# Performance work log

Measured on AMD Instinct MI355X. Metric: run time of the kernel, lower is better.

Reference implementation:

```python
import jax, jax.numpy as jnp
import numpy as np

N, E, F_IN, HID, HEADS, B, CLASSES = 50000, 800000, 128, 64, 4, 512, 2


def setup_inputs() -> dict:
    key = jax.random.key(0)
    ks = jax.random.split(key, 20)
    s = 0.05
    inp = {
        "x": jax.random.normal(ks[0], (N, F_IN), jnp.float32),
        "edge_index": jax.random.randint(ks[1], (2, E), 0, N, jnp.int32),
        "batch": jnp.sort(jax.random.randint(ks[2], (N,), 0, B, jnp.int32)),
        # GCN layers (3): layer0 F_IN->HID, layers 1,2 HID->HID
        "gcn_w0": jax.random.normal(ks[3], (F_IN, HID), jnp.float32) * s,
        "gcn_b0": jnp.zeros((HID,), jnp.float32),
        "gcn_w1": jax.random.normal(ks[4], (HID, HID), jnp.float32) * s,
        "gcn_b1": jnp.zeros((HID,), jnp.float32),
        "gcn_w2": jax.random.normal(ks[5], (HID, HID), jnp.float32) * s,
        "gcn_b2": jnp.zeros((HID,), jnp.float32),
        # GAT: W [HID, HEADS*HID], attention vectors [HEADS, HID], bias [HID] (concat=False)
        "gat_w": jax.random.normal(ks[6], (HID, HEADS * HID), jnp.float32) * s,
        "gat_att_src": jax.random.normal(ks[7], (HEADS, HID), jnp.float32) * s,
        "gat_att_dst": jax.random.normal(ks[8], (HEADS, HID), jnp.float32) * s,
        "gat_b": jnp.zeros((HID,), jnp.float32),
        # MLP head
        "lin1_w": jax.random.normal(ks[9], (HID, HID // 2), jnp.float32) * s,
        "lin1_b": jnp.zeros((HID // 2,), jnp.float32),
        "lin2_w": jax.random.normal(ks[10], (HID // 2, CLASSES), jnp.float32) * s,
        "lin2_b": jnp.zeros((CLASSES,), jnp.float32),
    }
    return inp


def _forward(x, edge_index, batch,
             gcn_w0, gcn_b0, gcn_w1, gcn_b1, gcn_w2, gcn_b2,
             gat_w, gat_att_src, gat_att_dst, gat_b,
             lin1_w, lin1_b, lin2_w, lin2_b):
    n = x.shape[0]
    loop = jnp.arange(n, dtype=edge_index.dtype)
    src = jnp.concatenate([edge_index[0], loop])  # [E+N] with self-loops
    dst = jnp.concatenate([edge_index[1], loop])

    # symmetric GCN normalization (self-loops included, deg >= 1)
    deg = jax.ops.segment_sum(jnp.ones_like(dst, dtype=x.dtype), dst, num_segments=n)
    dinv = jax.lax.rsqrt(jnp.maximum(deg, 1.0))
    norm = dinv[src] * dinv[dst]  # [E+N]

    for W, b in ((gcn_w0, gcn_b0), (gcn_w1, gcn_b1), (gcn_w2, gcn_b2)):
        h = x @ W  # [N, HID]
        x = jax.ops.segment_sum(h[src] * norm[:, None], dst, num_segments=n) + b
        x = jax.nn.relu(x)  # dropout is identity in eval mode

    # GAT layer (heads=HEADS, concat=False -> mean over heads)
    H, C = gat_att_src.shape
    h = (x @ gat_w).reshape(n, H, C)  # [N, H, C]
    a_src = jnp.einsum('nhc,hc->nh', h, gat_att_src)
    a_dst = jnp.einsum('nhc,hc->nh', h, gat_att_dst)
    e = jax.nn.leaky_relu(a_src[src] + a_dst[dst], 0.2)  # [E+N, H]
    m = jax.ops.segment_max(e, dst, num_segments=n)      # per-dst softmax max
    p = jnp.exp(e - m[dst])
    denom = jax.ops.segment_sum(p, dst, num_segments=n)
    alpha = p / denom[dst]                                # [E+N, H]
    out = jax.ops.segment_sum(h[src] * alpha[:, :, None], dst, num_segments=n)
    x = jax.nn.relu(out.mean(axis=1) + gat_b)             # [N, HID]

    # global mean pool + global max pool over graphs
    cnt = jax.ops.segment_sum(jnp.ones((n,), x.dtype), batch, num_segments=B)
    mean_p = jax.ops.segment_sum(x, batch, num_segments=B) / jnp.maximum(cnt, 1.0)[:, None]
    max_p = jax.ops.segment_max(x, batch, num_segments=B)
    max_p = jnp.where(cnt[:, None] > 0, max_p, 0.0)
    g = mean_p + max_p  # [B, HID]

    g = jax.nn.relu(g @ lin1_w + lin1_b)
    return g @ lin2_w + lin2_b  # [B, CLASSES]


def reference(x, edge_index, batch,
              gcn_w0, gcn_b0, gcn_w1, gcn_b1, gcn_w2, gcn_b2,
              gat_w, gat_att_src, gat_att_dst, gat_b,
              lin1_w, lin1_b, lin2_w, lin2_b):
    return _forward(x, edge_index, batch,
                    gcn_w0, gcn_b0, gcn_w1, gcn_b1, gcn_w2, gcn_b2,
                    gat_w, gat_att_src, gat_att_dst, gat_b,
                    lin1_w, lin1_b, lin2_w, lin2_b)
```

## Files before the change

kernel.cpp:

```cpp
#include <hip/hip_runtime.h>
#include <math.h>

typedef short bf8 __attribute__((ext_vector_type(8)));
typedef float f4 __attribute__((ext_vector_type(4)));
typedef unsigned short ushort_t;

#define BRANGE 128
#define NB_E 256

__device__ __forceinline__ float lanebcast(float v, int l) {
  return __int_as_float(__builtin_amdgcn_readlane(__float_as_int(v), l));
}
__device__ __forceinline__ int ilanebcast(int v, int l) {
  return __builtin_amdgcn_readlane(v, l);
}

__device__ __forceinline__ float wave_sum(float v) {
#pragma unroll
  for (int off = 32; off > 0; off >>= 1) v += __shfl_xor(v, off, 64);
  return v;
}

__device__ __forceinline__ ushort_t f2bf(float x) {
  unsigned int u = __float_as_uint(x);
  return (ushort_t)((u + 0x7fffu + ((u >> 16) & 1u)) >> 16);
}
__device__ __forceinline__ float b2f(ushort_t h) {
  return __uint_as_float(((unsigned int)h) << 16);
}


__global__ __launch_bounds__(256) void k_ehist(const int* __restrict__ dst,
                                               int* __restrict__ bhistT, int E, int nbuk) {
  __shared__ int h[512];
  int b = blockIdx.x, tid = threadIdx.x;
  for (int i = tid; i < nbuk; i += 256) h[i] = 0;
  __syncthreads();
  int chunk = (E + gridDim.x - 1) / gridDim.x;
  int e0 = b * chunk, e1 = min(E, e0 + chunk);
  for (int e = e0 + tid; e < e1; e += 256) atomicAdd(&h[dst[e] >> 7], 1);
  __syncthreads();
  for (int i = tid; i < nbuk; i += 256) bhistT[i * NB_E + b] = h[i];
}

__global__ __launch_bounds__(256) void k_btot(const int* __restrict__ bhistT,
                                              int* __restrict__ bcnt, int nb) {
  __shared__ int sm[256];
  int b = blockIdx.x, tid = threadIdx.x;
  sm[tid] = (tid < nb) ? bhistT[b * NB_E + tid] : 0;
  __syncthreads();
  for (int off = 128; off > 0; off >>= 1) {
    if (tid < off) sm[tid] += sm[tid + off];
    __syncthreads();
  }
  if (tid == 0) bcnt[b] = sm[0];
}

__global__ __launch_bounds__(512) void k_bscan(
    const int* __restrict__ bcnt, int* __restrict__ edgebase, int nbuk,
    int* __restrict__ rowstart, int n, int E) {
  __shared__ int smem[512];
  int t = threadIdx.x;
  int v = (t < nbuk) ? bcnt[t] : 0;
  smem[t] = v;
  __syncthreads();
  for (int off = 1; off < 512; off <<= 1) {
    int u = (t >= off) ? smem[t - off] : 0;
    __syncthreads();
    smem[t] += u;
    __syncthreads();
  }
  if (t < nbuk) edgebase[t] = smem[t] - v;
  if (t == 0) rowstart[n] = E + n;
}

__global__ __launch_bounds__(256) void k_bbase(int* __restrict__ bhistT,
                                               const int* __restrict__ edgebase,
                                               int nb) {
  __shared__ int sm[256];
  int b = blockIdx.x, tid = threadIdx.x;
  int v = (tid < nb) ? bhistT[b * NB_E + tid] : 0;
  sm[tid] = v;
  __syncthreads();
  for (int off = 1; off < 256; off <<= 1) {
    int u = (tid >= off) ? sm[tid - off] : 0;
    __syncthreads();
    sm[tid] += u;
    __syncthreads();
  }
  if (tid < nb) bhistT[b * NB_E + tid] = edgebase[b] + sm[tid] - v;
}

__global__ __launch_bounds__(256) void k_ebucket(
    const int* __restrict__ es, const int* __restrict__ ed,
    const int* __restrict__ bhistT, int* __restrict__ bedges, int E, int nbuk) {
  __shared__ int cur[512];
  int b = blockIdx.x, tid = threadIdx.x;
  for (int i = tid; i < nbuk; i += 256) cur[i] = bhistT[i * NB_E + b];
  __syncthreads();
  int chunk = (E + gridDim.x - 1) / gridDim.x;
  int e0 = b * chunk, e1 = min(E, e0 + chunk);
  for (int e = e0 + tid; e < e1; e += 256) {
    int s = es[e], d = ed[e];
    int pos = atomicAdd(&cur[d >> 7], 1);
    bedges[pos] = (s << 7) | (d & 127);
  }
}

__global__ __launch_bounds__(256) void k_ebsort(
    const int* __restrict__ bedges, const int* __restrict__ edgebase,
    const int* __restrict__ bcnt, int* __restrict__ colidx,
    int* __restrict__ rowstart, float* __restrict__ dinv, int n) {
  __shared__ int h[128];
  __shared__ int c[128];
  int b = blockIdx.x, tid = threadIdx.x;
  int nodes0 = b * BRANGE;
  int nnode = min(BRANGE, n - nodes0);
  int ebase = edgebase[b], ecnt = bcnt[b];
  int colbase = ebase + nodes0;
  if (tid < 128) h[tid] = (tid < nnode) ? 1 : 0;
  __syncthreads();
  for (int k = ebase + tid; k < ebase + ecnt; k += 256)
    atomicAdd(&h[bedges[k] & 127], 1);
  __syncthreads();
  int own = (tid < 128) ? h[tid] : 0;
  for (int off = 1; off < 128; off <<= 1) {
    int t = (tid >= off && tid < 128) ? h[tid - off] : 0;
    __syncthreads();
    if (tid < 128) h[tid] += t;
    __syncthreads();
  }
  if (tid < nnode) {
    int excl = h[tid] - own;
    int node = nodes0 + tid;
    rowstart[node] = colbase + excl;
    dinv[node] = 1.0f / sqrtf((float)own);
    colidx[colbase + excl] = node;
    c[tid] = excl + 1;
  }
  __syncthreads();
  for (int k = ebase + tid; k < ebase + ecnt; k += 256) {
    int p = bedges[k];
    int pos = atomicAdd(&c[p & 127], 1);
    colidx[colbase + pos] = p >> 7;
  }
}


__global__ void k_wswz0(const float* __restrict__ W, ushort_t* __restrict__ Bh,
                        ushort_t* __restrict__ Bl) {
  int e = blockIdx.x * 256 + threadIdx.x;
  if (e >= 4 * 4 * 64) return;
  int lane = e & 63, kc = (e >> 6) & 3, ct = e >> 8;
  int k0 = kc * 32 + (lane >> 4) * 8;
  int col = ct * 16 + (lane & 15);
#pragma unroll
  for (int j = 0; j < 8; j++) {
    float w = W[(k0 + j) * 64 + col];
    ushort_t h = f2bf(w);
    Bh[(size_t)e * 8 + j] = h;
    Bl[(size_t)e * 8 + j] = f2bf(w - b2f(h));
  }
}

__global__ void k_wswzg(const float* __restrict__ W, ushort_t* __restrict__ Bh,
                        ushort_t* __restrict__ Bl) {
  int e = blockIdx.x * 256 + threadIdx.x;
  if (e >= 4 * 8 * 64) return;
  int lane = e & 63, kc = (e >> 6) & 7, ct = e >> 9;
  int k0 = kc * 32 + (lane >> 4) * 8;
  int col = ct * 16 + (lane & 15);
#pragma unroll
  for (int j = 0; j < 8; j++) {
    int k = k0 + j;
    float w = W[(k & 63) * 256 + (k >> 6) * 64 + col];
    ushort_t h = f2bf(w);
    Bh[(size_t)e * 8 + j] = h;
    Bl[(size_t)e * 8 + j] = f2bf(w - b2f(h));
  }
}

__global__ __launch_bounds__(256) void k_gemm0_mfma(
    const float* __restrict__ X, const ushort_t* __restrict__ Bh,
    const ushort_t* __restrict__ Bl, const float* __restrict__ dinv,
    ushort_t* __restrict__ H, int n, int ntiles) {
  int tid = threadIdx.x, lane = tid & 63, wave = tid >> 6;
  int m = lane & 15, q = lane >> 4;
  for (int tile = blockIdx.x * 4 + wave; tile < ntiles; tile += gridDim.x * 4) {
    int ra = tile * 16 + m;
    if (ra >= n) ra = n - 1;
    const float* xrow = X + (size_t)ra * 128;
    f4 acc[4];
#pragma unroll
    for (int ct = 0; ct < 4; ct++) acc[ct] = (f4){0.f, 0.f, 0.f, 0.f};
#pragma unroll 2
    for (int kc = 0; kc < 4; kc++) {
      int ko = kc * 32 + q * 8;
      float4 xa = *(const float4*)(xrow + ko);
      float4 xb = *(const float4*)(xrow + ko + 4);
      float f[8] = {xa.x, xa.y, xa.z, xa.w, xb.x, xb.y, xb.z, xb.w};
      union { ushort_t u[8]; bf8 v; } Uh, Ul;
#pragma unroll
      for (int j = 0; j < 8; j++) {
        ushort_t h = f2bf(f[j]);
        Uh.u[j] = h;
        Ul.u[j] = f2bf(f[j] - b2f(h));
      }
#pragma unroll
      for (int ct = 0; ct < 4; ct++) {
        size_t boff = ((size_t)(ct * 4 + kc) * 64 + lane) * 8;
        bf8 bh = *(const bf8*)(Bh + boff);
        bf8 bl = *(const bf8*)(Bl + boff);
        acc[ct] = __builtin_amdgcn_mfma_f32_16x16x32_bf16(Uh.v, bh, acc[ct], 0, 0, 0);
        acc[ct] = __builtin_amdgcn_mfma_f32_16x16x32_bf16(Ul.v, bh, acc[ct], 0, 0, 0);
        acc[ct] = __builtin_amdgcn_mfma_f32_16x16x32_bf16(Uh.v, bl, acc[ct], 0, 0, 0);
      }
    }
#pragma unroll
    for (int r = 0; r < 4; r++) {
      int row = tile * 16 + q * 4 + r;
      if (row < n) {
        float dv = dinv[row];
#pragma unroll
        for (int ct = 0; ct < 4; ct++)
          H[(size_t)row * 64 + ct * 16 + m] = f2bf(acc[ct][r] * dv);
      }
    }
  }
}

__device__ __forceinline__ float gather_sum(const ushort_t* __restrict__ h_in,
                                            const int* __restrict__ colidx,
                                            int s0, int s1, int lane) {
  float acc = 0.0f, accB = 0.0f;
  for (int base = s0; base < s1; base += 64) {
    int cnt = min(64, s1 - base);
    int myidx = (lane < cnt) ? colidx[base + lane] : 0;
    int k = 0;
    for (; k + 3 < cnt; k += 4) {
      int sa = ilanebcast(myidx, k);
      int sb = ilanebcast(myidx, k + 1);
      int sc = ilanebcast(myidx, k + 2);
      int sd = ilanebcast(myidx, k + 3);
      float va = b2f(h_in[(size_t)sa * 64 + lane]);
      float vb = b2f(h_in[(size_t)sb * 64 + lane]);
      float vc = b2f(h_in[(size_t)sc * 64 + lane]);
      float vd = b2f(h_in[(size_t)sd * 64 + lane]);
      acc += va; accB += vb; acc += vc; accB += vd;
    }
    for (; k < cnt; k++) {
      int sa = ilanebcast(myidx, k);
      acc += b2f(h_in[(size_t)sa * 64 + lane]);
    }
  }
  return acc + accB;
}

__global__ __launch_bounds__(256) void k_agg_gemm(
    const ushort_t* __restrict__ h_in, const float* __restrict__ dinv,
    const int* __restrict__ rowstart, const int* __restrict__ colidx,
    const float* __restrict__ bias, const float* __restrict__ Wn,
    ushort_t* __restrict__ h_out, int n) {
  __shared__ float lds_w[64 * 64];
  int tid = threadIdx.x;
  for (int idx = tid; idx < 64 * 64; idx += 256) lds_w[idx] = Wn[idx];
  __syncthreads();
  int lane = tid & 63;
  float bv = bias[lane];
  int gw = blockIdx.x * 4 + (tid >> 6);
  int nw = gridDim.x * 4;
  for (int node = gw; node < n; node += nw) {
    int s0 = rowstart[node], s1 = rowstart[node + 1];
    float acc = gather_sum(h_in, colidx, s0, s1, lane);
    float dvn = dinv[node];
    float x1 = fmaxf(fmaf(dvn, acc, bv), 0.0f);
    float o = 0.0f;
#pragma unroll 8
    for (int k = 0; k < 64; k++)
      o = fmaf(lanebcast(x1, k), lds_w[k * 64 + lane], o);
    h_out[(size_t)node * 64 + lane] = f2bf(o * dvn);
  }
}

__global__ __launch_bounds__(256) void k_agg_gatpre(
    const ushort_t* __restrict__ h_in, const float* __restrict__ dinv,
    const int* __restrict__ rowstart, const int* __restrict__ colidx,
    const float* __restrict__ bias,
    const float* __restrict__ q_src, const float* __restrict__ q_dst,
    ushort_t* __restrict__ x3, float* __restrict__ a_src, float* __restrict__ a_dst,
    int n) {
  int tid = threadIdx.x;
  int lane = tid & 63;
  float bv = bias[lane];
  float qs[4], qd[4];
#pragma unroll
  for (int h = 0; h < 4; h++) {
    qs[h] = q_src[h * 64 + lane];
    qd[h] = q_dst[h * 64 + lane];
  }
  int gw = blockIdx.x * 4 + (tid >> 6);
  int nw = gridDim.x * 4;
  for (int node = gw; node < n; node += nw) {
    int s0 = rowstart[node], s1 = rowstart[node + 1];
    float acc = gather_sum(h_in, colidx, s0, s1, lane);
    float xv = fmaxf(fmaf(dinv[node], acc, bv), 0.0f);
    x3[(size_t)node * 64 + lane] = f2bf(xv);
    float ps[4], pd[4];
#pragma unroll
    for (int h = 0; h < 4; h++) {
      ps[h] = wave_sum(xv * qs[h]);
      pd[h] = wave_sum(xv * qd[h]);
    }
    if (lane == 0) {
      *(float4*)&a_src[(size_t)node * 4] = make_float4(ps[0], ps[1], ps[2], ps[3]);
      *(float4*)&a_dst[(size_t)node * 4] = make_float4(pd[0], pd[1], pd[2], pd[3]);
    }
  }
}

__global__ void k_qpre(const float* __restrict__ W, const float* __restrict__ att_s,
                       const float* __restrict__ att_d,
                       float* __restrict__ q_src, float* __restrict__ q_dst) {
  int t = threadIdx.x;
  int h = t >> 6, k = t & 63;
  float ss = 0.0f, sd = 0.0f;
  for (int c = 0; c < 64; c++) {
    float w = W[k * 256 + h * 64 + c];
    ss = fmaf(w, att_s[h * 64 + c], ss);
    sd = fmaf(w, att_d[h * 64 + c], sd);
  }
  q_src[h * 64 + k] = ss;
  q_dst[h * 64 + k] = sd;
}

__global__ __launch_bounds__(256) void k_gat_gather(
    const ushort_t* __restrict__ x3, const float* __restrict__ a_src,
    const float* __restrict__ a_dst, const int* __restrict__ rowstart,
    const int* __restrict__ colidx, ushort_t* __restrict__ Ahi,
    ushort_t* __restrict__ Alo, int n) {
  int node = (blockIdx.x * blockDim.x + threadIdx.x) >> 6;
  int lane = threadIdx.x & 63;
  if (node >= n) return;
  const float4 adv = *(const float4*)&a_dst[(size_t)node * 4];
  int s0 = rowstart[node], s1 = rowstart[node + 1];
  float acc0 = 0, acc1 = 0, acc2 = 0, acc3 = 0;
  float S0 = 0, S1 = 0, S2 = 0, S3 = 0;
  for (int base = s0; base < s1; base += 64) {
    int cnt = min(64, s1 - base);
    bool act = (lane < cnt);
    int myidx = act ? colidx[base + lane] : 0;
    float w0 = 0, w1 = 0, w2 = 0, w3 = 0;
    if (act) {
      const float4 as = *(const float4*)&a_src[(size_t)myidx * 4];
      float e0 = as.x + adv.x; e0 = (e0 > 0.f) ? e0 : 0.2f * e0; w0 = __expf(e0);
      float e1 = as.y + adv.y; e1 = (e1 > 0.f) ? e1 : 0.2f * e1; w1 = __expf(e1);
      float e2 = as.z + adv.z; e2 = (e2 > 0.f) ? e2 : 0.2f * e2; w2 = __expf(e2);
      float e3 = as.w + adv.w; e3 = (e3 > 0.f) ? e3 : 0.2f * e3; w3 = __expf(e3);
    }
    S0 += wave_sum(w0); S1 += wave_sum(w1);
    S2 += wave_sum(w2); S3 += wave_sum(w3);
    int k = 0;
    for (; k + 1 < cnt; k += 2) {
      int sa = ilanebcast(myidx, k);
      int sb = ilanebcast(myidx, k + 1);
      float wa0 = lanebcast(w0, k), wb0 = lanebcast(w0, k + 1);
      float wa1 = lanebcast(w1, k), wb1 = lanebcast(w1, k + 1);
      float wa2 = lanebcast(w2, k), wb2 = lanebcast(w2, k + 1);
      float wa3 = lanebcast(w3, k), wb3 = lanebcast(w3, k + 1);
      float va = b2f(x3[(size_t)sa * 64 + lane]);
      float vb = b2f(x3[(size_t)sb * 64 + lane]);
      acc0 = fmaf(wa0, va, acc0); acc1 = fmaf(wa1, va, acc1);
      acc2 = fmaf(wa2, va, acc2); acc3 = fmaf(wa3, va, acc3);
      acc0 = fmaf(wb0, vb, acc0); acc1 = fmaf(wb1, vb, acc1);
      acc2 = fmaf(wb2, vb, acc2); acc3 = fmaf(wb3, vb, acc3);
    }
    if (k < cnt) {
      int sa = ilanebcast(myidx, k);
      float wa0 = lanebcast(w0, k), wa1 = lanebcast(w1, k);
      float wa2 = lanebcast(w2, k), wa3 = lanebcast(w3, k);
      float va = b2f(x3[(size_t)sa * 64 + lane]);
      acc0 = fmaf(wa0, va, acc0); acc1 = fmaf(wa1, va, acc1);
      acc2 = fmaf(wa2, va, acc2); acc3 = fmaf(wa3, va, acc3);
    }
  }
  float v[4] = {acc0 * (0.25f / S0), acc1 * (0.25f / S1),
                acc2 * (0.25f / S2), acc3 * (0.25f / S3)};
  size_t baseo = (size_t)node * 256 + lane;
#pragma unroll
  for (int h = 0; h < 4; h++) {
    ushort_t hb = f2bf(v[h]);
    Ahi[baseo + h * 64] = hb;
    Alo[baseo + h * 64] = f2bf(v[h] - b2f(hb));
  }
}

__global__ __launch_bounds__(256) void k_gat_proj_mfma(
    const ushort_t* __restrict__ Ahi, const ushort_t* __restrict__ Alo,
    const ushort_t* __restrict__ Bh, const ushort_t* __restrict__ Bl,
    const float* __restrict__ bias, float* __restrict__ out, int n, int ntiles) {
  int tid = threadIdx.x, lane = tid & 63, wave = tid >> 6;
  int m = lane & 15, q = lane >> 4;
  float bv[4];
#pragma unroll
  for (int ct = 0; ct < 4; ct++) bv[ct] = bias[ct * 16 + m];
  for (int tile = blockIdx.x * 4 + wave; tile < ntiles; tile += gridDim.x * 4) {
    int ra = tile * 16 + m;
    if (ra >= n) ra = n - 1;
    const ushort_t* ahr = Ahi + (size_t)ra * 256;
    const ushort_t* alr = Alo + (size_t)ra * 256;
    f4 acc[4];
#pragma unroll
    for (int ct = 0; ct < 4; ct++) acc[ct] = (f4){0.f, 0.f, 0.f, 0.f};
#pragma unroll 2
    for (int kc = 0; kc < 8; kc++) {
      int ko = kc * 32 + q * 8;
      bf8 ah = *(const bf8*)(ahr + ko);
      bf8 al = *(const bf8*)(alr + ko);
#pragma unroll
      for (int ct = 0; ct < 4; ct++) {
        size_t boff = ((size_t)(ct * 8 + kc) * 64 + lane) * 8;
        bf8 bh = *(const bf8*)(Bh + boff);
        bf8 bl = *(const bf8*)(Bl + boff);
        acc[ct] = __builtin_amdgcn_mfma_f32_16x16x32_bf16(ah, bh, acc[ct], 0, 0, 0);
        acc[ct] = __builtin_amdgcn_mfma_f32_16x16x32_bf16(al, bh, acc[ct], 0, 0, 0);
        acc[ct] = __builtin_amdgcn_mfma_f32_16x16x32_bf16(ah, bl, acc[ct], 0, 0, 0);
      }
    }
#pragma unroll
    for (int r = 0; r < 4; r++) {
      int row = tile * 16 + q * 4 + r;
      if (row < n) {
#pragma unroll
        for (int ct = 0; ct < 4; ct++)
          out[(size_t)row * 64 + ct * 16 + m] = fmaxf(acc[ct][r] + bv[ct], 0.f);
      }
    }
  }
}

__global__ void k_gstart(const int* __restrict__ batch, int* gs, int n, int B) {
  int g = blockIdx.x * blockDim.x + threadIdx.x;
  if (g > B) return;
  int lo = 0, hi = n;
  while (lo < hi) {
    int mid = (lo + hi) >> 1;
    if (batch[mid] < g) lo = mid + 1; else hi = mid;
  }
  gs[g] = lo;
}

__global__ __launch_bounds__(256) void k_pool(const float* __restrict__ x,
                                              const int* __restrict__ gs,
                                              float* __restrict__ gvec, int B) {
  int g = (blockIdx.x * blockDim.x + threadIdx.x) >> 6;
  int lane = threadIdx.x & 63;
  if (g >= B) return;
  int s0 = gs[g], s1 = gs[g + 1];
  float sum = 0.0f, mx = -INFINITY;
  for (int nd = s0; nd < s1; ++nd) {
    float v = x[(size_t)nd * 64 + lane];
    sum += v;
    mx = fmaxf(mx, v);
  }
  int cnt = s1 - s0;
  float mean = sum / fmaxf((float)cnt, 1.0f);
  float mp = (cnt > 0) ? mx : 0.0f;
  gvec[g * 64 + lane] = mean + mp;
}

__global__ __launch_bounds__(256) void k_mlp(const float* __restrict__ gvec,
                                             const float* __restrict__ w1,
                                             const float* __restrict__ b1,
                                             const float* __restrict__ w2,
                                             const float* __restrict__ b2,
                                             float* __restrict__ out, int B) {
  int g = blockIdx.x * blockDim.x + threadIdx.x;
  if (g >= B) return;
  float gv[64];
#pragma unroll
  for (int i = 0; i < 64; i++) gv[i] = gvec[g * 64 + i];
  float o0 = b2[0], o1 = b2[1];
  for (int j = 0; j < 32; j++) {
    float a = b1[j];
#pragma unroll
    for (int i = 0; i < 64; i++) a = fmaf(gv[i], w1[i * 32 + j], a);
    a = fmaxf(a, 0.0f);
    o0 = fmaf(a, w2[j * 2 + 0], o0);
    o1 = fmaf(a, w2[j * 2 + 1], o1);
  }
  out[g * 2 + 0] = o0;
  out[g * 2 + 1] = o1;
}

extern "C" void kernel_launch(void* const* d_in, const int* in_sizes, int n_in,
                              void* d_out, int out_size, void* d_ws, size_t ws_size,
                              hipStream_t stream) {
  const float* x     = (const float*)d_in[0];
  const int*   ei    = (const int*)d_in[1];
  const int*   batch = (const int*)d_in[2];
  const float* w0 = (const float*)d_in[3];  const float* b0 = (const float*)d_in[4];
  const float* w1 = (const float*)d_in[5];  const float* b1 = (const float*)d_in[6];
  const float* w2 = (const float*)d_in[7];  const float* b2 = (const float*)d_in[8];
  const float* gat_w = (const float*)d_in[9];
  const float* att_s = (const float*)d_in[10];
  const float* att_d = (const float*)d_in[11];
  const float* gat_b = (const float*)d_in[12];
  const float* l1w = (const float*)d_in[13]; const float* l1b = (const float*)d_in[14];
  const float* l2w = (const float*)d_in[15]; const float* l2b = (const float*)d_in[16];

  const int N = in_sizes[0] / 128;
  const int E = in_sizes[1] / 2;
  const int B = out_size / 2;
  const int NT = (N + 15) / 16;
  const int NBUK = (N + BRANGE - 1) / BRANGE;

  char* ws = (char*)d_ws;
  size_t off = 0;
  auto alloc = [&](size_t bytes) -> void* {
    void* p = ws + off;
    off = (off + bytes + 255) & ~(size_t)255;
    return p;
  };
  int*      bhistT   = (int*)alloc((size_t)NBUK * NB_E * 4);
  int*      edgebase = (int*)alloc((size_t)NBUK * 4);
  int*      bcnt     = (int*)alloc((size_t)NBUK * 4);
  int*      bedges   = (int*)alloc((size_t)E * 4);
  int*      rowstart = (int*)alloc((size_t)(N + 1) * 4);
  int*      colidx   = (int*)alloc((size_t)(E + N) * 4);
  float*    dinv     = (float*)alloc((size_t)N * 4);
  ushort_t* hbuf     = (ushort_t*)alloc((size_t)N * 64 * 2);
  ushort_t* hbuf2    = (ushort_t*)alloc((size_t)N * 64 * 2);
  ushort_t* xg       = (ushort_t*)alloc((size_t)N * 64 * 2);
  float*    gatout   = (float*)alloc((size_t)N * 64 * 4);
  ushort_t* Ahi      = (ushort_t*)alloc((size_t)N * 256 * 2);
  ushort_t* Alo      = (ushort_t*)alloc((size_t)N * 256 * 2);
  float*    a_src    = (float*)alloc((size_t)N * 4 * 4);
  float*    a_dst    = (float*)alloc((size_t)N * 4 * 4);
  float*    q_src    = (float*)alloc(4 * 64 * 4);
  float*    q_dst    = (float*)alloc(4 * 64 * 4);
  ushort_t* B0h      = (ushort_t*)alloc(4 * 4 * 64 * 8 * 2);
  ushort_t* B0l      = (ushort_t*)alloc(4 * 4 * 64 * 8 * 2);
  ushort_t* Bgh      = (ushort_t*)alloc(4 * 8 * 64 * 8 * 2);
  ushort_t* Bgl      = (ushort_t*)alloc(4 * 8 * 64 * 8 * 2);
  int*      gs       = (int*)alloc((size_t)(B + 1) * 4);
  float*    gvec     = (float*)alloc((size_t)B * 64 * 4);
  (void)ws_size; (void)n_in;

  k_ehist<<<NB_E, 256, 0, stream>>>(ei + E, bhistT, E, NBUK);
  k_btot<<<NBUK, 256, 0, stream>>>(bhistT, bcnt, NB_E);
  k_bscan<<<1, 512, 0, stream>>>(bcnt, edgebase, NBUK, rowstart, N, E);
  k_bbase<<<NBUK, 256, 0, stream>>>(bhistT, edgebase, NB_E);
  k_ebucket<<<NB_E, 256, 0, stream>>>(ei, ei + E, bhistT, bedges, E, NBUK);
  k_ebsort<<<NBUK, 256, 0, stream>>>(bedges, edgebase, bcnt, colidx, rowstart, dinv, N);
  k_qpre<<<1, 256, 0, stream>>>(gat_w, att_s, att_d, q_src, q_dst);
  k_wswz0<<<4, 256, 0, stream>>>(w0, B0h, B0l);
  k_wswzg<<<8, 256, 0, stream>>>(gat_w, Bgh, Bgl);

  const int AGB = 2048;
  k_gemm0_mfma<<<1024, 256, 0, stream>>>(x, B0h, B0l, dinv, hbuf, N, NT);
  k_agg_gemm<<<AGB, 256, 0, stream>>>(hbuf, dinv, rowstart, colidx, b0, w1, hbuf2, N);
  k_agg_gemm<<<AGB, 256, 0, stream>>>(hbuf2, dinv, rowstart, colidx, b1, w2, hbuf, N);
  k_agg_gatpre<<<AGB, 256, 0, stream>>>(hbuf, dinv, rowstart, colidx, b2,
                                        q_src, q_dst, xg, a_src, a_dst, N);
  k_gat_gather<<<(N + 3) / 4, 256, 0, stream>>>(xg, a_src, a_dst, rowstart, colidx,
                                                Ahi, Alo, N);
  k_gat_proj_mfma<<<1024, 256, 0, stream>>>(Ahi, Alo, Bgh, Bgl, gat_b, gatout, N, NT);
  k_gstart<<<(B + 1 + 255) / 256, 256, 0, stream>>>(batch, gs, N, B);
  k_pool<<<(B + 3) / 4, 256, 0, stream>>>(gatout, gs, gvec, B);
  k_mlp<<<(B + 255) / 256, 256, 0, stream>>>(gvec, l1w, l1b, l2w, l2b, (float*)d_out, B);
}
```

Baseline: 388.2 us.

## Switch hidden activations to fp16 with packed gathers and MFMA per-node GEMMs

Intermediate GCN activations move from bf16 to fp16. Neighbor gathers now load packed half2 values, with the two half-waves each taking alternate edges and combining at the end. The per-node 64x64 weight multiply, formerly a readlane-broadcast FMA loop, now stages 16 aggregated rows in LDS and runs fp16 MFMA with split hi/lo weights. The GAT attention-logit dot products use one MFMA instead of wave reductions, and the GAT gather uses the same half-wave packed layout with attention weights held in LDS. Accumulating the aggregation in fp16 and storing activations in fp16 lowers precision and risks overflow. Processing 16 serial nodes per wave may also reduce latency hiding.

```diff
diff --git a/kernel.cpp b/kernel.cpp
--- a/kernel.cpp
+++ b/kernel.cpp
@@ -2,15 +2,15 @@
 #include <math.h>
 
 typedef short bf8 __attribute__((ext_vector_type(8)));
+typedef _Float16 h8 __attribute__((ext_vector_type(8)));
+typedef _Float16 h2v __attribute__((ext_vector_type(2)));
 typedef float f4 __attribute__((ext_vector_type(4)));
+typedef float f2v __attribute__((ext_vector_type(2)));
 typedef unsigned short ushort_t;
 
 #define BRANGE 128
 #define NB_E 256
 
-__device__ __forceinline__ float lanebcast(float v, int l) {
-  return __int_as_float(__builtin_amdgcn_readlane(__float_as_int(v), l));
-}
 __device__ __forceinline__ int ilanebcast(int v, int l) {
   return __builtin_amdgcn_readlane(v, l);
 }
@@ -28,7 +28,6 @@
 __device__ __forceinline__ float b2f(ushort_t h) {
   return __uint_as_float(((unsigned int)h) << 16);
 }
-
 
 __global__ __launch_bounds__(256) void k_ehist(const int* __restrict__ dst,
                                                int* __restrict__ bhistT, int E, int nbuk) {
@@ -163,6 +162,22 @@
   }
 }
 
+__global__ void k_wswz1(const float* __restrict__ W, _Float16* __restrict__ Bh,
+                        _Float16* __restrict__ Bl) {
+  int e = blockIdx.x * 256 + threadIdx.x;
+  if (e >= 8 * 64) return;
+  int lane = e & 63, kc = (e >> 6) & 1, ct = e >> 7;
+  int k0 = kc * 32 + (lane >> 4) * 8;
+  int col = ct * 16 + (lane & 15);
+#pragma unroll
+  for (int j = 0; j < 8; j++) {
+    float w = W[(k0 + j) * 64 + col];
+    _Float16 h = (_Float16)w;
+    Bh[(size_t)e * 8 + j] = h;
+    Bl[(size_t)e * 8 + j] = (_Float16)(w - (float)h);
+  }
+}
+
 __global__ void k_wswzg(const float* __restrict__ W, ushort_t* __restrict__ Bh,
                         ushort_t* __restrict__ Bl) {
   int e = blockIdx.x * 256 + threadIdx.x;
@@ -177,144 +192,6 @@
     ushort_t h = f2bf(w);
     Bh[(size_t)e * 8 + j] = h;
     Bl[(size_t)e * 8 + j] = f2bf(w - b2f(h));
-  }
-}
-
-__global__ __launch_bounds__(256) void k_gemm0_mfma(
-    const float* __restrict__ X, const ushort_t* __restrict__ Bh,
-    const ushort_t* __restrict__ Bl, const float* __restrict__ dinv,
-    ushort_t* __restrict__ H, int n, int ntiles) {
-  int tid = threadIdx.x, lane = tid & 63, wave = tid >> 6;
-  int m = lane & 15, q = lane >> 4;
-  for (int tile = blockIdx.x * 4 + wave; tile < ntiles; tile += gridDim.x * 4) {
-    int ra = tile * 16 + m;
-    if (ra >= n) ra = n - 1;
-    const float* xrow = X + (size_t)ra * 128;
-    f4 acc[4];
-#pragma unroll
-    for (int ct = 0; ct < 4; ct++) acc[ct] = (f4){0.f, 0.f, 0.f, 0.f};
-#pragma unroll 2
-    for (int kc = 0; kc < 4; kc++) {
-      int ko = kc * 32 + q * 8;
-      float4 xa = *(const float4*)(xrow + ko);
-      float4 xb = *(const float4*)(xrow + ko + 4);
-      float f[8] = {xa.x, xa.y, xa.z, xa.w, xb.x, xb.y, xb.z, xb.w};
-      union { ushort_t u[8]; bf8 v; } Uh, Ul;
-#pragma unroll
-      for (int j = 0; j < 8; j++) {
-        ushort_t h = f2bf(f[j]);
-        Uh.u[j] = h;
-        Ul.u[j] = f2bf(f[j] - b2f(h));
-      }
-#pragma unroll
-      for (int ct = 0; ct < 4; ct++) {
-        size_t boff = ((size_t)(ct * 4 + kc) * 64 + lane) * 8;
-        bf8 bh = *(const bf8*)(Bh + boff);
-        bf8 bl = *(const bf8*)(Bl + boff);
-        acc[ct] = __builtin_amdgcn_mfma_f32_16x16x32_bf16(Uh.v, bh, acc[ct], 0, 0, 0);
-        acc[ct] = __builtin_amdgcn_mfma_f32_16x16x32_bf16(Ul.v, bh, acc[ct], 0, 0, 0);
-        acc[ct] = __builtin_amdgcn_mfma_f32_16x16x32_bf16(Uh.v, bl, acc[ct], 0, 0, 0);
-      }
-    }
-#pragma unroll
-    for (int r = 0; r < 4; r++) {
-      int row = tile * 16 + q * 4 + r;
-      if (row < n) {
-        float dv = dinv[row];
-#pragma unroll
-        for (int ct = 0; ct < 4; ct++)
-          H[(size_t)row * 64 + ct * 16 + m] = f2bf(acc[ct][r] * dv);
-      }
-    }
-  }
-}
-
-__device__ __forceinline__ float gather_sum(const ushort_t* __restrict__ h_in,
-                                            const int* __restrict__ colidx,
-                                            int s0, int s1, int lane) {
-  float acc = 0.0f, accB = 0.0f;
-  for (int base = s0; base < s1; base += 64) {
-    int cnt = min(64, s1 - base);
-    int myidx = (lane < cnt) ? colidx[base + lane] : 0;
-    int k = 0;
-    for (; k + 3 < cnt; k += 4) {
-      int sa = ilanebcast(myidx, k);
-      int sb = ilanebcast(myidx, k + 1);
-      int sc = ilanebcast(myidx, k + 2);
-      int sd = ilanebcast(myidx, k + 3);
-      float va = b2f(h_in[(size_t)sa * 64 + lane]);
-      float vb = b2f(h_in[(size_t)sb * 64 + lane]);
-      float vc = b2f(h_in[(size_t)sc * 64 + lane]);
-      float vd = b2f(h_in[(size_t)sd * 64 + lane]);
-      acc += va; accB += vb; acc += vc; accB += vd;
-    }
-    for (; k < cnt; k++) {
-      int sa = ilanebcast(myidx, k);
-      acc += b2f(h_in[(size_t)sa * 64 + lane]);
-    }
-  }
-  return acc + accB;
-}
-
-__global__ __launch_bounds__(256) void k_agg_gemm(
-    const ushort_t* __restrict__ h_in, const float* __restrict__ dinv,
-    const int* __restrict__ rowstart, const int* __restrict__ colidx,
-    const float* __restrict__ bias, const float* __restrict__ Wn,
-    ushort_t* __restrict__ h_out, int n) {
-  __shared__ float lds_w[64 * 64];
-  int tid = threadIdx.x;
-  for (int idx = tid; idx < 64 * 64; idx += 256) lds_w[idx] = Wn[idx];
-  __syncthreads();
-  int lane = tid & 63;
-  float bv = bias[lane];
-  int gw = blockIdx.x * 4 + (tid >> 6);
-  int nw = gridDim.x * 4;
-  for (int node = gw; node < n; node += nw) {
-    int s0 = rowstart[node], s1 = rowstart[node + 1];
-    float acc = gather_sum(h_in, colidx, s0, s1, lane);
-    float dvn = dinv[node];
-    float x1 = fmaxf(fmaf(dvn, acc, bv), 0.0f);
-    float o = 0.0f;
-#pragma unroll 8
-    for (int k = 0; k < 64; k++)
-      o = fmaf(lanebcast(x1, k), lds_w[k * 64 + lane], o);
-    h_out[(size_t)node * 64 + lane] = f2bf(o * dvn);
-  }
-}
-
-__global__ __launch_bounds__(256) void k_agg_gatpre(
-    const ushort_t* __restrict__ h_in, const float* __restrict__ dinv,
-    const int* __restrict__ rowstart, const int* __restrict__ colidx,
-    const float* __restrict__ bias,
-    const float* __restrict__ q_src, const float* __restrict__ q_dst,
-    ushort_t* __restrict__ x3, float* __restrict__ a_src, float* __restrict__ a_dst,
-    int n) {
-  int tid = threadIdx.x;
-  int lane = tid & 63;
-  float bv = bias[lane];
-  float qs[4], qd[4];
-#pragma unroll
-  for (int h = 0; h < 4; h++) {
-    qs[h] = q_src[h * 64 + lane];
-    qd[h] = q_dst[h * 64 + lane];
-  }
-  int gw = blockIdx.x * 4 + (tid >> 6);
-  int nw = gridDim.x * 4;
-  for (int node = gw; node < n; node += nw) {
-    int s0 = rowstart[node], s1 = rowstart[node + 1];
-    float acc = gather_sum(h_in, colidx, s0, s1, lane);
-    float xv = fmaxf(fmaf(dinv[node], acc, bv), 0.0f);
-    x3[(size_t)node * 64 + lane] = f2bf(xv);
-    float ps[4], pd[4];
-#pragma unroll
-    for (int h = 0; h < 4; h++) {
-      ps[h] = wave_sum(xv * qs[h]);
-      pd[h] = wave_sum(xv * qd[h]);
-    }
-    if (lane == 0) {
-      *(float4*)&a_src[(size_t)node * 4] = make_float4(ps[0], ps[1], ps[2], ps[3]);
-      *(float4*)&a_dst[(size_t)node * 4] = make_float4(pd[0], pd[1], pd[2], pd[3]);
-    }
   }
 }
 
@@ -333,17 +210,212 @@
   q_dst[h * 64 + k] = sd;
 }
 
+__global__ void k_qswz(const float* __restrict__ q_src, const float* __restrict__ q_dst,
+                       _Float16* __restrict__ Bq) {
+  int e = threadIdx.x;
+  if (e >= 128) return;
+  int lane = e & 63, kc = e >> 6;
+  int k0 = kc * 32 + (lane >> 4) * 8;
+  int col = lane & 15;
+#pragma unroll
+  for (int j = 0; j < 8; j++) {
+    int k = k0 + j;
+    float v = (col < 4) ? q_src[col * 64 + k]
+                        : ((col < 8) ? q_dst[(col - 4) * 64 + k] : 0.0f);
+    Bq[(size_t)e * 8 + j] = (_Float16)v;
+  }
+}
+
+__global__ __launch_bounds__(256) void k_gemm0_mfma(
+    const float* __restrict__ X, const ushort_t* __restrict__ Bh,
+    const ushort_t* __restrict__ Bl, const float* __restrict__ dinv,
+    _Float16* __restrict__ H, int n, int ntiles) {
+  int tid = threadIdx.x, lane = tid & 63, wave = tid >> 6;
+  int m = lane & 15, q = lane >> 4;
+  for (int tile = blockIdx.x * 4 + wave; tile < ntiles; tile += gridDim.x * 4) {
+    int ra = tile * 16 + m;
+    if (ra >= n) ra = n - 1;
+    const float* xrow = X + (size_t)ra * 128;
+    f4 acc[4];
+#pragma unroll
+    for (int ct = 0; ct < 4; ct++) acc[ct] = (f4){0.f, 0.f, 0.f, 0.f};
+#pragma unroll 2
+    for (int kc = 0; kc < 4; kc++) {
+      int ko = kc * 32 + q * 8;
+      float4 xa = *(const float4*)(xrow + ko);
+      float4 xb = *(const float4*)(xrow + ko + 4);
+      float f[8] = {xa.x, xa.y, xa.z, xa.w, xb.x, xb.y, xb.z, xb.w};
+      union { ushort_t u[8]; bf8 v; } Uh, Ul;
+#pragma unroll
+      for (int j = 0; j < 8; j++) {
+        ushort_t h = f2bf(f[j]);
+        Uh.u[j] = h;
+        Ul.u[j] = f2bf(f[j] - b2f(h));
+      }
+#pragma unroll
+      for (int ct = 0; ct < 4; ct++) {
+        size_t boff = ((size_t)(ct * 4 + kc) * 64 + lane) * 8;
+        bf8 bh = *(const bf8*)(Bh + boff);
+        bf8 bl = *(const bf8*)(Bl + boff);
+        acc[ct] = __builtin_amdgcn_mfma_f32_16x16x32_bf16(Uh.v, bh, acc[ct], 0, 0, 0);
+        acc[ct] = __builtin_amdgcn_mfma_f32_16x16x32_bf16(Ul.v, bh, acc[ct], 0, 0, 0);
+        acc[ct] = __builtin_amdgcn_mfma_f32_16x16x32_bf16(Uh.v, bl, acc[ct], 0, 0, 0);
+      }
+    }
+#pragma unroll
+    for (int r = 0; r < 4; r++) {
+      int row = tile * 16 + q * 4 + r;
+      if (row < n) {
+        float dv = dinv[row];
+#pragma unroll
+        for (int ct = 0; ct < 4; ct++)
+          H[(size_t)row * 64 + ct * 16 + m] = (_Float16)(acc[ct][r] * dv);
+      }
+    }
+  }
+}
+
+__device__ __forceinline__ f2v gather_packed(const _Float16* __restrict__ h_in,
+                                             const int* __restrict__ colidx,
+                                             int s0, int s1, int lane, int p, int c2) {
+  h2v acc = {(_Float16)0.f, (_Float16)0.f};
+  for (int base = s0; base < s1; base += 64) {
+    int cnt = min(64, s1 - base);
+    int myidx = (lane < cnt) ? colidx[base + lane] : 0;
+    int k = 0;
+    for (; k + 1 < cnt; k += 2) {
+      int s = __shfl(myidx, k + p);
+      h2v hv = *(const h2v*)(h_in + ((size_t)s << 6) + 2 * c2);
+      acc += hv;
+    }
+    if (k < cnt) {
+      int s = ilanebcast(myidx, k);
+      if (p == 0) {
+        h2v hv = *(const h2v*)(h_in + ((size_t)s << 6) + 2 * c2);
+        acc += hv;
+      }
+    }
+  }
+  unsigned int au;
+  __builtin_memcpy(&au, &acc, 4);
+  unsigned int bu = (unsigned int)__shfl_xor((int)au, 32);
+  h2v other;
+  __builtin_memcpy(&other, &bu, 4);
+  acc += other;
+  f2v r = {(float)acc.x, (float)acc.y};
+  return r;
+}
+
+__global__ __launch_bounds__(256) void k_agg_gemm_mfma(
+    const _Float16* __restrict__ h_in, const float* __restrict__ dinv,
+    const int* __restrict__ rowstart, const int* __restrict__ colidx,
+    const float* __restrict__ bias, const _Float16* __restrict__ Bh,
+    const _Float16* __restrict__ Bl, _Float16* __restrict__ h_out,
+    int n, int ntiles) {
+  __shared__ __align__(16) _Float16 xstage[4][16][64];
+  int tid = threadIdx.x, lane = tid & 63, w = tid >> 6;
+  int p = lane >> 5, c2 = lane & 31;
+  int m = lane & 15, q = lane >> 4;
+  f2v bias2 = {bias[2 * c2], bias[2 * c2 + 1]};
+  for (int tile = blockIdx.x * 4 + w; tile < ntiles; tile += gridDim.x * 4) {
+    for (int i = 0; i < 16; i++) {
+      int node = tile * 16 + i;
+      h2v hx = {(_Float16)0.f, (_Float16)0.f};
+      if (node < n) {
+        int s0 = rowstart[node], s1 = rowstart[node + 1];
+        f2v a = gather_packed(h_in, colidx, s0, s1, lane, p, c2);
+        float dvn = dinv[node];
+        hx.x = (_Float16)fmaxf(fmaf(dvn, a.x, bias2.x), 0.f);
+        hx.y = (_Float16)fmaxf(fmaf(dvn, a.y, bias2.y), 0.f);
+      }
+      if (lane < 32) *(h2v*)&xstage[w][i][2 * c2] = hx;
+    }
+    h8 af0 = *(const h8*)&xstage[w][m][q * 8];
+    h8 af1 = *(const h8*)&xstage[w][m][32 + q * 8];
+    f4 acc[4];
+#pragma unroll
+    for (int ct = 0; ct < 4; ct++) {
+      acc[ct] = (f4){0.f, 0.f, 0.f, 0.f};
+      size_t o0 = ((size_t)(ct * 2 + 0) * 64 + lane) * 8;
+      size_t o1 = ((size_t)(ct * 2 + 1) * 64 + lane) * 8;
+      h8 bh0 = *(const h8*)(Bh + o0);
+      h8 bh1 = *(const h8*)(Bh + o1);
+      h8 bl0 = *(const h8*)(Bl + o0);
+      h8 bl1 = *(const h8*)(Bl + o1);
+      acc[ct] = __builtin_amdgcn_mfma_f32_16x16x32_f16(af0, bh0, acc[ct], 0, 0, 0);
+      acc[ct] = __builtin_amdgcn_mfma_f32_16x16x32_f16(af1, bh1, acc[ct], 0, 0, 0);
+      acc[ct] = __builtin_amdgcn_mfma_f32_16x16x32_f16(af0, bl0, acc[ct], 0, 0, 0);
+      acc[ct] = __builtin_amdgcn_mfma_f32_16x16x32_f16(af1, bl1, acc[ct], 0, 0, 0);
+    }
+#pragma unroll
+    for (int r = 0; r < 4; r++) {
+      int node = tile * 16 + q * 4 + r;
+      if (node < n) {
+        float dv = dinv[node];
+#pragma unroll
+        for (int ct = 0; ct < 4; ct++)
+          h_out[(size_t)node * 64 + ct * 16 + m] = (_Float16)(acc[ct][r] * dv);
+      }
+    }
+  }
+}
+
+__global__ __launch_bounds__(256) void k_agg_gatpre_mfma(
+    const _Float16* __restrict__ h_in, const float* __restrict__ dinv,
+    const int* __restrict__ rowstart, const int* __restrict__ colidx,
+    const float* __restrict__ bias, const _Float16* __restrict__ Bq,
+    _Float16* __restrict__ x3, float* __restrict__ a_src, float* __restrict__ a_dst,
+    int n, int ntiles) {
+  __shared__ __align__(16) _Float16 xstage[4][16][64];
+  int tid = threadIdx.x, lane = tid & 63, w = tid >> 6;
+  int p = lane >> 5, c2 = lane & 31;
+  int m = lane & 15, q = lane >> 4;
+  f2v bias2 = {bias[2 * c2], bias[2 * c2 + 1]};
+  for (int tile = blockIdx.x * 4 + w; tile < ntiles; tile += gridDim.x * 4) {
+    for (int i = 0; i < 16; i++) {
+      int node = tile * 16 + i;
+      h2v hx = {(_Float16)0.f, (_Float16)0.f};
+      if (node < n) {
+        int s0 = rowstart[node], s1 = rowstart[node + 1];
+        f2v a = gather_packed(h_in, colidx, s0, s1, lane, p, c2);
+        float dvn = dinv[node];
+        hx.x = (_Float16)fmaxf(fmaf(dvn, a.x, bias2.x), 0.f);
+        hx.y = (_Float16)fmaxf(fmaf(dvn, a.y, bias2.y), 0.f);
+        if (lane < 32) *(h2v*)(x3 + ((size_t)node << 6) + 2 * c2) = hx;
+      }
+      if (lane < 32) *(h2v*)&xstage[w][i][2 * c2] = hx;
+    }
+    h8 af0 = *(const h8*)&xstage[w][m][q * 8];
+    h8 af1 = *(const h8*)&xstage[w][m][32 + q * 8];
+    h8 bq0 = *(const h8*)(Bq + (size_t)lane * 8);
+    h8 bq1 = *(const h8*)(Bq + ((size_t)(64 + lane)) * 8);
+    f4 accL = (f4){0.f, 0.f, 0.f, 0.f};
+    accL = __builtin_amdgcn_mfma_f32_16x16x32_f16(af0, bq0, accL, 0, 0, 0);
+    accL = __builtin_amdgcn_mfma_f32_16x16x32_f16(af1, bq1, accL, 0, 0, 0);
+#pragma unroll
+    for (int r = 0; r < 4; r++) {
+      int node = tile * 16 + q * 4 + r;
+      if (node < n) {
+        if (m < 4) a_src[(size_t)node * 4 + m] = accL[r];
+        else if (m < 8) a_dst[(size_t)node * 4 + (m - 4)] = accL[r];
+      }
+    }
+  }
+}
+
 __global__ __launch_bounds__(256) void k_gat_gather(
-    const ushort_t* __restrict__ x3, const float* __restrict__ a_src,
+    const _Float16* __restrict__ x3, const float* __restrict__ a_src,
     const float* __restrict__ a_dst, const int* __restrict__ rowstart,
     const int* __restrict__ colidx, ushort_t* __restrict__ Ahi,
     ushort_t* __restrict__ Alo, int n) {
-  int node = (blockIdx.x * blockDim.x + threadIdx.x) >> 6;
-  int lane = threadIdx.x & 63;
+  __shared__ __align__(16) float4 wlds[4][64];
+  int tid = threadIdx.x, lane = tid & 63, w = tid >> 6;
+  int p = lane >> 5, c2 = lane & 31;
+  int node = blockIdx.x * 4 + w;
   if (node >= n) return;
   const float4 adv = *(const float4*)&a_dst[(size_t)node * 4];
   int s0 = rowstart[node], s1 = rowstart[node + 1];
-  float acc0 = 0, acc1 = 0, acc2 = 0, acc3 = 0;
+  f2v acc0 = {0.f, 0.f}, acc1 = {0.f, 0.f}, acc2 = {0.f, 0.f}, acc3 = {0.f, 0.f};
   float S0 = 0, S1 = 0, S2 = 0, S3 = 0;
   for (int base = s0; base < s1; base += 64) {
     int cnt = min(64, s1 - base);
@@ -359,39 +431,51 @@
     }
     S0 += wave_sum(w0); S1 += wave_sum(w1);
     S2 += wave_sum(w2); S3 += wave_sum(w3);
+    wlds[w][lane] = make_float4(w0, w1, w2, w3);
     int k = 0;
     for (; k + 1 < cnt; k += 2) {
-      int sa = ilanebcast(myidx, k);
-      int sb = ilanebcast(myidx, k + 1);
-      float wa0 = lanebcast(w0, k), wb0 = lanebcast(w0, k + 1);
-      float wa1 = lanebcast(w1, k), wb1 = lanebcast(w1, k + 1);
-      float wa2 = lanebcast(w2, k), wb2 = lanebcast(w2, k + 1);
-      float wa3 = lanebcast(w3, k), wb3 = lanebcast(w3, k + 1);
-      float va = b2f(x3[(size_t)sa * 64 + lane]);
-      float vb = b2f(x3[(size_t)sb * 64 + lane]);
-      acc0 = fmaf(wa0, va, acc0); acc1 = fmaf(wa1, va, acc1);
-      acc2 = fmaf(wa2, va, acc2); acc3 = fmaf(wa3, va, acc3);
-      acc0 = fmaf(wb0, vb, acc0); acc1 = fmaf(wb1, vb, acc1);
-      acc2 = fmaf(wb2, vb, acc2); acc3 = fmaf(wb3, vb, acc3);
+      int s = __shfl(myidx, k + p);
+      float4 wv = wlds[w][k + p];
+      h2v hv = *(const h2v*)(x3 + ((size_t)s << 6) + 2 * c2);
+      f2v xv = {(float)hv.x, (float)hv.y};
+      acc0.x = fmaf(wv.x, xv.x, acc0.x); acc0.y = fmaf(wv.x, xv.y, acc0.y);
+      acc1.x = fmaf(wv.y, xv.x, acc1.x); acc1.y = fmaf(wv.y, xv.y, acc1.y);
+      acc2.x = fmaf(wv.z, xv.x, acc2.x); acc2.y = fmaf(wv.z, xv.y, acc2.y);
+      acc3.x = fmaf(wv.w, xv.x, acc3.x); acc3.y = fmaf(wv.w, xv.y, acc3.y);
     }
     if (k < cnt) {
-      int sa = ilanebcast(myidx, k);
-      float wa0 = lanebcast(w0, k), wa1 = lanebcast(w1, k);
-      float wa2 = lanebcast(w2, k), wa3 = lanebcast(w3, k);
-      float va = b2f(x3[(size_t)sa * 64 + lane]);
-      acc0 = fmaf(wa0, va, acc0); acc1 = fmaf(wa1, va, acc1);
-      acc2 = fmaf(wa2, va, acc2); acc3 = fmaf(wa3, va, acc3);
-    }
-  }
-  float v[4] = {acc0 * (0.25f / S0), acc1 * (0.25f / S1),
-                acc2 * (0.25f / S2), acc3 * (0.25f / S3)};
-  size_t baseo = (size_t)node * 256 + lane;
-#pragma unroll
-  for (int h = 0; h < 4; h++) {
-    ushort_t hb = f2bf(v[h]);
-    Ahi[baseo + h * 64] = hb;
-    Alo[baseo + h * 64] = f2bf(v[h] - b2f(hb));
-  }
+      if (p == 0) {
+        float4 wv = wlds[w][k];
+        int s = ilanebcast(myidx, k);
+        h2v hv = *(const h2v*)(x3 + ((size_t)s << 6) + 2 * c2);
+        f2v xv = {(float)hv.x, (float)hv.y};
+        acc0.x = fmaf(wv.x, xv.x, acc0.x); acc0.y = fmaf(wv.x, xv.y, acc0.y);
+        acc1.x = fmaf(wv.y, xv.x, acc1.x); acc1.y = fmaf(wv.y, xv.y, acc1.y);
+        acc2.x = fmaf(wv.z, xv.x, acc2.x); acc2.y = fmaf(wv.z, xv.y, acc2.y);
+        acc3.x = fmaf(wv.w, xv.x, acc3.x); acc3.y = fmaf(wv.w, xv.y, acc3.y);
+      }
+    }
+  }
+  acc0.x += __shfl_xor(acc0.x, 32); acc0.y += __shfl_xor(acc0.y, 32);
+  acc1.x += __shfl_xor(acc1.x, 32); acc1.y += __shfl_xor(acc1.y, 32);
+  acc2.x += __shfl_xor(acc2.x, 32); acc2.y += __shfl_xor(acc2.y, 32);
+  acc3.x += __shfl_xor(acc3.x, 32); acc3.y += __shfl_xor(acc3.y, 32);
+  float r0 = 0.25f / S0, r1 = 0.25f / S1, r2 = 0.25f / S2, r3 = 0.25f / S3;
+  acc0.x *= r0; acc0.y *= r0; acc1.x *= r1; acc1.y *= r1;
+  acc2.x *= r2; acc2.y *= r2; acc3.x *= r3; acc3.y *= r3;
+  f2v va = (p == 0) ? acc0 : acc2;
+  f2v vb = (p == 0) ? acc1 : acc3;
+  ushort_t ha0 = f2bf(va.x), ha1 = f2bf(va.y);
+  ushort_t la0 = f2bf(va.x - b2f(ha0)), la1 = f2bf(va.y - b2f(ha1));
+  ushort_t hb0 = f2bf(vb.x), hb1 = f2bf(vb.y);
+  ushort_t lb0 = f2bf(vb.x - b2f(hb0)), lb1 = f2bf(vb.y - b2f(hb1));
+  unsigned int* AhiU = (unsigned int*)Ahi;
+  unsigned int* AloU = (unsigned int*)Alo;
+  size_t bi = (size_t)node * 128 + (size_t)(2 * p) * 32 + c2;
+  AhiU[bi] = (unsigned int)ha0 | ((unsigned int)ha1 << 16);
+  AloU[bi] = (unsigned int)la0 | ((unsigned int)la1 << 16);
+  AhiU[bi + 32] = (unsigned int)hb0 | ((unsigned int)hb1 << 16);
+  AloU[bi + 32] = (unsigned int)lb0 | ((unsigned int)lb1 << 16);
 }
 
 __global__ __launch_bounds__(256) void k_gat_proj_mfma(
@@ -521,29 +605,34 @@
     off = (off + bytes + 255) & ~(size_t)255;
     return p;
   };
-  int*      bhistT   = (int*)alloc((size_t)NBUK * NB_E * 4);
-  int*      edgebase = (int*)alloc((size_t)NBUK * 4);
-  int*      bcnt     = (int*)alloc((size_t)NBUK * 4);
-  int*      bedges   = (int*)alloc((size_t)E * 4);
-  int*      rowstart = (int*)alloc((size_t)(N + 1) * 4);
-  int*      colidx   = (int*)alloc((size_t)(E + N) * 4);
-  float*    dinv     = (float*)alloc((size_t)N * 4);
-  ushort_t* hbuf     = (ushort_t*)alloc((size_t)N * 64 * 2);
-  ushort_t* hbuf2    = (ushort_t*)alloc((size_t)N * 64 * 2);
-  ushort_t* xg       = (ushort_t*)alloc((size_t)N * 64 * 2);
-  float*    gatout   = (float*)alloc((size_t)N * 64 * 4);
-  ushort_t* Ahi      = (ushort_t*)alloc((size_t)N * 256 * 2);
-  ushort_t* Alo      = (ushort_t*)alloc((size_t)N * 256 * 2);
-  float*    a_src    = (float*)alloc((size_t)N * 4 * 4);
-  float*    a_dst    = (float*)alloc((size_t)N * 4 * 4);
-  float*    q_src    = (float*)alloc(4 * 64 * 4);
-  float*    q_dst    = (float*)alloc(4 * 64 * 4);
-  ushort_t* B0h      = (ushort_t*)alloc(4 * 4 * 64 * 8 * 2);
-  ushort_t* B0l      = (ushort_t*)alloc(4 * 4 * 64 * 8 * 2);
-  ushort_t* Bgh      = (ushort_t*)alloc(4 * 8 * 64 * 8 * 2);
-  ushort_t* Bgl      = (ushort_t*)alloc(4 * 8 * 64 * 8 * 2);
-  int*      gs       = (int*)alloc((size_t)(B + 1) * 4);
-  float*    gvec     = (float*)alloc((size_t)B * 64 * 4);
+  int*       bhistT   = (int*)alloc((size_t)NBUK * NB_E * 4);
+  int*       edgebase = (int*)alloc((size_t)NBUK * 4);
+  int*       bcnt     = (int*)alloc((size_t)NBUK * 4);
+  int*       bedges   = (int*)alloc((size_t)E * 4);
+  int*       rowstart = (int*)alloc((size_t)(N + 1) * 4);
+  int*       colidx   = (int*)alloc((size_t)(E + N) * 4);
+  float*     dinv     = (float*)alloc((size_t)N * 4);
+  _Float16*  hbuf     = (_Float16*)alloc((size_t)N * 64 * 2);
+  _Float16*  hbuf2    = (_Float16*)alloc((size_t)N * 64 * 2);
+  _Float16*  xg       = (_Float16*)alloc((size_t)N * 64 * 2);
+  float*     gatout   = (float*)alloc((size_t)N * 64 * 4);
+  ushort_t*  Ahi      = (ushort_t*)alloc((size_t)N * 256 * 2);
+  ushort_t*  Alo      = (ushort_t*)alloc((size_t)N * 256 * 2);
+  float*     a_src    = (float*)alloc((size_t)N * 4 * 4);
+  float*     a_dst    = (float*)alloc((size_t)N * 4 * 4);
+  float*     q_src    = (float*)alloc(4 * 64 * 4);
+  float*     q_dst    = (float*)alloc(4 * 64 * 4);
+  ushort_t*  B0h      = (ushort_t*)alloc(4 * 4 * 64 * 8 * 2);
+  ushort_t*  B0l      = (ushort_t*)alloc(4 * 4 * 64 * 8 * 2);
+  _Float16*  Bw1h     = (_Float16*)alloc(8 * 64 * 8 * 2);
+  _Float16*  Bw1l     = (_Float16*)alloc(8 * 64 * 8 * 2);
+  _Float16*  Bw2h     = (_Float16*)alloc(8 * 64 * 8 * 2);
+  _Float16*  Bw2l     = (_Float16*)alloc(8 * 64 * 8 * 2);
+  _Float16*  Bq       = (_Float16*)alloc(2 * 64 * 8 * 2);
+  ushort_t*  Bgh      = (ushort_t*)alloc(4 * 8 * 64 * 8 * 2);
+  ushort_t*  Bgl      = (ushort_t*)alloc(4 * 8 * 64 * 8 * 2);
+  int*       gs       = (int*)alloc((size_t)(B + 1) * 4);
+  float*     gvec     = (float*)alloc((size_t)B * 64 * 4);
   (void)ws_size; (void)n_in;
 
   k_ehist<<<NB_E, 256, 0, stream>>>(ei + E, bhistT, E, NBUK);
@@ -553,15 +642,20 @@
   k_ebucket<<<NB_E, 256, 0, stream>>>(ei, ei + E, bhistT, bedges, E, NBUK);
   k_ebsort<<<NBUK, 256, 0, stream>>>(bedges, edgebase, bcnt, colidx, rowstart, dinv, N);
   k_qpre<<<1, 256, 0, stream>>>(gat_w, att_s, att_d, q_src, q_dst);
+  k_qswz<<<1, 256, 0, stream>>>(q_src, q_dst, Bq);
   k_wswz0<<<4, 256, 0, stream>>>(w0, B0h, B0l);
+  k_wswz1<<<2, 256, 0, stream>>>(w1, Bw1h, Bw1l);
+  k_wswz1<<<2, 256, 0, stream>>>(w2, Bw2h, Bw2l);
   k_wswzg<<<8, 256, 0, stream>>>(gat_w, Bgh, Bgl);
 
-  const int AGB = 2048;
+  const int AGB = (NT + 3) / 4;
   k_gemm0_mfma<<<1024, 256, 0, stream>>>(x, B0h, B0l, dinv, hbuf, N, NT);
-  k_agg_gemm<<<AGB, 256, 0, stream>>>(hbuf, dinv, rowstart, colidx, b0, w1, hbuf2, N);
-  k_agg_gemm<<<AGB, 256, 0, stream>>>(hbuf2, dinv, rowstart, colidx, b1, w2, hbuf, N);
-  k_agg_gatpre<<<AGB, 256, 0, stream>>>(hbuf, dinv, rowstart, colidx, b2,
-                                        q_src, q_dst, xg, a_src, a_dst, N);
+  k_agg_gemm_mfma<<<AGB, 256, 0, stream>>>(hbuf, dinv, rowstart, colidx, b0,
+                                           Bw1h, Bw1l, hbuf2, N, NT);
+  k_agg_gemm_mfma<<<AGB, 256, 0, stream>>>(hbuf2, dinv, rowstart, colidx, b1,
+                                           Bw2h, Bw2l, hbuf, N, NT);
+  k_agg_gatpre_mfma<<<AGB, 256, 0, stream>>>(hbuf, dinv, rowstart, colidx, b2,
+                                             Bq, xg, a_src, a_dst, N, NT);
   k_gat_gather<<<(N + 3) / 4, 256, 0, stream>>>(xg, a_src, a_dst, rowstart, colidx,
                                                 Ahi, Alo, N);
   k_gat_proj_mfma<<<1024, 256, 0, stream>>>(Ahi, Alo, Bgh, Bgl, gat_b, gatout, N, NT);
```

Measured after the change: 477.6 us. +23.0%, slower.
